# Optimization experiments

Measured on AMD Instinct MI355X. Metric: run time of the kernel, lower is better.

The kernel has to match this reference:

```python
import jax, jax.numpy as jnp
import numpy as np

MIN_SIGMA = 0.001


def setup_inputs() -> dict:
    key = jax.random.key(0)
    kA, kB = jax.random.split(key)
    A = jax.random.normal(kA, (8, 2048, 128), dtype=jnp.float32)
    B = jax.random.normal(kB, (4096, 128), dtype=jnp.float32)
    sigma = jnp.float32(1.0)
    return {"A": A, "B": B, "sigma": sigma}


def reference(A, B, sigma):
    # A: (bs, n, d), B: (m, d) -> K: (bs, n, m)
    A_norm = jnp.sum(A * A, axis=-1, keepdims=True)          # (bs, n, 1)
    B_norm = jnp.sum(B * B, axis=-1)[None, None, :]          # (1, 1, m)
    AB = jnp.einsum('bnd,md->bnm', A, B)                     # (bs, n, m)
    dist2 = jnp.maximum(A_norm + B_norm - 2.0 * AB, 0.0)
    sig = jnp.maximum(sigma, MIN_SIGMA)
    K = jnp.exp(-dist2 / (2.0 * sig * sig))
    return K
```

## Files before the change

### kernel.cpp

```cpp
#include <hip/hip_runtime.h>


typedef __attribute__((ext_vector_type(8))) short bf16x8;
typedef __attribute__((ext_vector_type(4))) float f32x4;

#define NROW_A 16384
#define NROW_B 4096
#define D      128

#define OFF_AHI 0u
#define OFF_BHI (OFF_AHI + NROW_A * D * 2u)
#define OFF_NA  (OFF_BHI + NROW_B * D * 2u)
#define OFF_NB  (OFF_NA + NROW_A * 4u)
#define WS_NEED (OFF_NB + NROW_B * 4u)

#define BAR_LDS() do { asm volatile("s_waitcnt lgkmcnt(0)" ::: "memory"); \
                       __builtin_amdgcn_s_barrier(); } while (0)

__device__ __forceinline__ short f2bf_hi(float x) {
    union { float f; unsigned u; } v; v.f = x;
    unsigned r = (v.u + 0x7fffu + ((v.u >> 16) & 1u)) >> 16;
    return (short)r;
}
__device__ __forceinline__ float bf2f(short h) {
    union { unsigned u; float f; } v; v.u = ((unsigned)(unsigned short)h) << 16;
    return v.f;
}

__global__ __launch_bounds__(256)
void rbf_precompute(const float* __restrict__ A, const float* __restrict__ Bm,
                    short* __restrict__ Ahi, short* __restrict__ Bhi,
                    float* __restrict__ nA, float* __restrict__ nB) {
    const int g   = blockIdx.x * 256 + threadIdx.x;
    const int row = g >> 4;
    const int c   = g & 15;

    const float* src; short* dhi; float* nrm; int r;
    if (row < NROW_A) {
        r = row; src = A + (size_t)r * D;
        dhi = Ahi + (size_t)r * D; nrm = nA + r;
    } else {
        r = row - NROW_A; src = Bm + (size_t)r * D;
        dhi = Bhi + (size_t)r * D; nrm = nB + r;
    }

    float4 v0 = *(const float4*)(src + c * 8);
    float4 v1 = *(const float4*)(src + c * 8 + 4);
    float f[8] = {v0.x, v0.y, v0.z, v0.w, v1.x, v1.y, v1.z, v1.w};

    bf16x8 hi;
    float ss = 0.0f;
#pragma unroll
    for (int e = 0; e < 8; ++e) {
        hi[e] = f2bf_hi(f[e]);
        ss += f[e] * f[e];
    }
    *(bf16x8*)(dhi + c * 8) = hi;

#pragma unroll
    for (int m = 1; m <= 8; m <<= 1) ss += __shfl_xor(ss, m);
    if (c == 0) *nrm = ss;
}

__global__ __launch_bounds__(512, 4)
void rbf_mfma_persist(const short* __restrict__ Ahi, const short* __restrict__ Bhi,
                      const float* __restrict__ nAg, const float* __restrict__ nBg,
                      const float* __restrict__ sigp, float* __restrict__ out) {
    __shared__ __align__(16) short sA[128 * 128];
    __shared__ __align__(16) short sB[128 * 128];

    const int tid = threadIdx.x;
    const int bid = blockIdx.x;
    const int xcd = bid & 7;
    const int idx = bid >> 3;
    const int bcol = ((xcd << 2) + (idx & 3)) << 7;
    const int bg   = idx >> 2;

    const int srow = tid >> 2;
    const int sc4  = tid & 3;

    const int lane = tid & 63;
    const int w    = tid >> 6;
    const int wr   = (w >> 1) << 5;
    const int wc   = (w & 1) << 6;
    const int lr   = lane & 15;
    const int kb   = lane >> 4;

#pragma unroll
    for (int it = 0; it < 4; ++it) {
        const int c  = sc4 + (it << 2);
        const int cs = c ^ (srow & 15);
        *(bf16x8*)&sB[srow * 128 + cs * 8] =
            *(const bf16x8*)&Bhi[(size_t)(bcol + srow) * D + c * 8];
    }
    const int brow0 = (bg << 3) << 7;
#pragma unroll
    for (int it = 0; it < 4; ++it) {
        const int c  = sc4 + (it << 2);
        const int cs = c ^ (srow & 15);
        *(bf16x8*)&sA[srow * 128 + cs * 8] =
            *(const bf16x8*)&Ahi[(size_t)(brow0 + srow) * D + c * 8];
    }

    f32x4 nb[4];
#pragma unroll
    for (int j = 0; j < 4; ++j)
        nb[j] = *(const f32x4*)&nBg[bcol + wc + (j << 4) + (kb << 2)];

    float nac0 = nAg[brow0 + wr + lr];
    float nac1 = nAg[brow0 + wr + 16 + lr];

    float sg = fmaxf(sigp[0], 0.001f);
    const float cc = -0.5f / (sg * sg);

    __syncthreads();

    bf16x8 rh[4];
    float nan0 = 0.0f, nan1 = 0.0f;

    for (int t = 0; t < 8; ++t) {
        const int browt = ((bg << 3) + t) << 7;

        if (t < 7) {
            const int brn = browt + 128;
            nan0 = nAg[brn + wr + lr];
            nan1 = nAg[brn + wr + 16 + lr];
#pragma unroll
            for (int it = 0; it < 4; ++it) {
                const int c = sc4 + (it << 2);
                rh[it] = *(const bf16x8*)&Ahi[(size_t)(brn + srow) * D + c * 8];
            }
        }

        f32x4 acc[2][4] = {};
#pragma unroll
        for (int ks = 0; ks < 4; ++ks) {
            const int off = (((ks << 2) + kb) ^ lr) << 3;
            bf16x8 af[2], bf[4];
#pragma unroll
            for (int i = 0; i < 2; ++i)
                af[i] = *(const bf16x8*)&sA[(wr + (i << 4) + lr) * 128 + off];
#pragma unroll
            for (int j = 0; j < 4; ++j)
                bf[j] = *(const bf16x8*)&sB[(wc + (j << 4) + lr) * 128 + off];
#pragma unroll
            for (int i = 0; i < 2; ++i)
#pragma unroll
                for (int j = 0; j < 4; ++j)
                    acc[i][j] = __builtin_amdgcn_mfma_f32_16x16x32_bf16(bf[j], af[i], acc[i][j], 0, 0, 0);
        }

#pragma unroll
        for (int i = 0; i < 2; ++i) {
            const int orow = browt + wr + (i << 4) + lr;
            const float na = i ? nac1 : nac0;
#pragma unroll
            for (int j = 0; j < 4; ++j) {
                const int ocol = wc + (j << 4) + (kb << 2);
                f32x4 v;
#pragma unroll
                for (int r = 0; r < 4; ++r) {
                    float d2 = fmaxf(na + nb[j][r] - 2.0f * acc[i][j][r], 0.0f);
                    v[r] = __expf(d2 * cc);
                }
                *(f32x4*)(out + (size_t)orow * 4096 + bcol + ocol) = v;
            }
        }

        if (t < 7) {
            BAR_LDS();
#pragma unroll
            for (int it = 0; it < 4; ++it) {
                const int c  = sc4 + (it << 2);
                const int cs = c ^ (srow & 15);
                *(bf16x8*)&sA[srow * 128 + cs * 8] = rh[it];
            }
            BAR_LDS();
            nac0 = nan0;
            nac1 = nan1;
        }
    }
}

#define PK 136
__global__ __launch_bounds__(256, 2)
void rbf_mfma_fallback(const float* __restrict__ A, const float* __restrict__ Bm,
                       const float* __restrict__ sigp, float* __restrict__ out) {
    __shared__ __align__(16) short sAhi[64 * PK];
    __shared__ __align__(16) short sAlo[64 * PK];
    __shared__ __align__(16) short sBhi[64 * PK];
    __shared__ __align__(16) short sBlo[64 * PK];
    __shared__ float nA[64];
    __shared__ float nB[64];

    const int tid  = threadIdx.x;
    const int brow = blockIdx.y << 6;
    const int bcol = blockIdx.x << 6;

    const int r0 = tid >> 5;
    const int kq = (tid & 31) << 2;
#pragma unroll
    for (int it = 0; it < 8; ++it) {
        const int row = r0 + (it << 3);
        const float4 va = *(const float4*)(A  + (size_t)(brow + row) * 128 + kq);
        const float4 vb = *(const float4*)(Bm + (size_t)(bcol + row) * 128 + kq);
        short4 ha, la, hb, lb;
        ha.x = f2bf_hi(va.x); la.x = f2bf_hi(va.x - bf2f(ha.x));
        ha.y = f2bf_hi(va.y); la.y = f2bf_hi(va.y - bf2f(ha.y));
        ha.z = f2bf_hi(va.z); la.z = f2bf_hi(va.z - bf2f(ha.z));
        ha.w = f2bf_hi(va.w); la.w = f2bf_hi(va.w - bf2f(ha.w));
        hb.x = f2bf_hi(vb.x); lb.x = f2bf_hi(vb.x - bf2f(hb.x));
        hb.y = f2bf_hi(vb.y); lb.y = f2bf_hi(vb.y - bf2f(hb.y));
        hb.z = f2bf_hi(vb.z); lb.z = f2bf_hi(vb.z - bf2f(hb.z));
        hb.w = f2bf_hi(vb.w); lb.w = f2bf_hi(vb.w - bf2f(hb.w));
        const int idx = row * PK + kq;
        *(short4*)(&sAhi[idx]) = ha;
        *(short4*)(&sAlo[idx]) = la;
        *(short4*)(&sBhi[idx]) = hb;
        *(short4*)(&sBlo[idx]) = lb;
        float sa = va.x * va.x + va.y * va.y + va.z * va.z + va.w * va.w;
        float sb = vb.x * vb.x + vb.y * vb.y + vb.z * vb.z + vb.w * vb.w;
#pragma unroll
        for (int m = 16; m >= 1; m >>= 1) { sa += __shfl_xor(sa, m); sb += __shfl_xor(sb, m); }
        if ((tid & 31) == 0) { nA[row] = sa; nB[row] = sb; }
    }
    __syncthreads();

    const int lane = tid & 63;
    const int w    = tid >> 6;
    const int wr   = (w >> 1) << 5;
    const int wc   = (w & 1) << 5;
    const int lr   = lane & 15;
    const int kb   = lane >> 4;
    f32x4 acc[2][2] = {};
#pragma unroll
    for (int ks = 0; ks < 4; ++ks) {
        const int kc = (ks << 5) + (kb << 3);
        bf16x8 ahi[2], alo[2], bhi[2], blo[2];
#pragma unroll
        for (int i = 0; i < 2; ++i) {
            const int ar = (wr + (i << 4) + lr) * PK + kc;
            ahi[i] = *(const bf16x8*)(&sAhi[ar]);
            alo[i] = *(const bf16x8*)(&sAlo[ar]);
            const int br = (wc + (i << 4) + lr) * PK + kc;
            bhi[i] = *(const bf16x8*)(&sBhi[br]);
            blo[i] = *(const bf16x8*)(&sBlo[br]);
        }
#pragma unroll
        for (int i = 0; i < 2; ++i)
#pragma unroll
            for (int j = 0; j < 2; ++j) {
                acc[i][j] = __builtin_amdgcn_mfma_f32_16x16x32_bf16(ahi[i], bhi[j], acc[i][j], 0, 0, 0);
                acc[i][j] = __builtin_amdgcn_mfma_f32_16x16x32_bf16(ahi[i], blo[j], acc[i][j], 0, 0, 0);
                acc[i][j] = __builtin_amdgcn_mfma_f32_16x16x32_bf16(alo[i], bhi[j], acc[i][j], 0, 0, 0);
            }
    }
    float sg = fmaxf(sigp[0], 0.001f);
    const float c = -0.5f / (sg * sg);
#pragma unroll
    for (int i = 0; i < 2; ++i)
#pragma unroll
        for (int j = 0; j < 2; ++j)
#pragma unroll
            for (int r = 0; r < 4; ++r) {
                const int lrow = wr + (i << 4) + (kb << 2) + r;
                const int lcol = wc + (j << 4) + lr;
                float d2 = nA[lrow] + nB[lcol] - 2.0f * acc[i][j][r];
                d2 = fmaxf(d2, 0.0f);
                out[(size_t)(brow + lrow) * 4096 + (bcol + lcol)] = __expf(d2 * c);
            }
}

extern "C" void kernel_launch(void* const* d_in, const int* in_sizes, int n_in,
                              void* d_out, int out_size, void* d_ws, size_t ws_size,
                              hipStream_t stream) {
    const float* A    = (const float*)d_in[0];
    const float* Bm   = (const float*)d_in[1];
    const float* sigp = (const float*)d_in[2];
    float* out = (float*)d_out;

    if (ws_size >= WS_NEED) {
        char* ws = (char*)d_ws;
        short* Ahi = (short*)(ws + OFF_AHI);
        short* Bhi = (short*)(ws + OFF_BHI);
        float* nA  = (float*)(ws + OFF_NA);
        float* nB  = (float*)(ws + OFF_NB);

        dim3 pgrid((NROW_A + NROW_B) * 16 / 256, 1, 1);
        rbf_precompute<<<pgrid, 256, 0, stream>>>(A, Bm, Ahi, Bhi, nA, nB);

        rbf_mfma_persist<<<dim3(512, 1, 1), dim3(512, 1, 1), 0, stream>>>(
            Ahi, Bhi, nA, nB, sigp, out);
    } else {
        dim3 grid(4096 / 64, 16384 / 64, 1);
        rbf_mfma_fallback<<<grid, dim3(256, 1, 1), 0, stream>>>(A, Bm, sigp, out);
    }
}
```

Before: 60.75 us.

## Load A fragments directly from global into registers, drop A LDS staging

The persistent MFMA kernel no longer stages A tiles through shared memory. Each wave now loads its own A fragments straight from global memory into registers, prefetching the next tile right after the MFMAs. This removes the per-tile LDS writes and both barriers, and halves LDS use, which may allow higher occupancy. In exchange, A rows read by several waves are fetched redundantly from global/L2, and the prefetch now overwrites the fragment registers after the MFMA loop, so less of the load latency is hidden.

```diff
diff --git a/kernel.cpp b/kernel.cpp
--- a/kernel.cpp
+++ b/kernel.cpp
@@ -13,9 +13,6 @@
 #define OFF_NA  (OFF_BHI + NROW_B * D * 2u)
 #define OFF_NB  (OFF_NA + NROW_A * 4u)
 #define WS_NEED (OFF_NB + NROW_B * 4u)
-
-#define BAR_LDS() do { asm volatile("s_waitcnt lgkmcnt(0)" ::: "memory"); \
-                       __builtin_amdgcn_s_barrier(); } while (0)
 
 __device__ __forceinline__ short f2bf_hi(float x) {
     union { float f; unsigned u; } v; v.f = x;
@@ -66,7 +63,6 @@
 void rbf_mfma_persist(const short* __restrict__ Ahi, const short* __restrict__ Bhi,
                       const float* __restrict__ nAg, const float* __restrict__ nBg,
                       const float* __restrict__ sigp, float* __restrict__ out) {
-    __shared__ __align__(16) short sA[128 * 128];
     __shared__ __align__(16) short sB[128 * 128];
 
     const int tid = threadIdx.x;
@@ -93,20 +89,20 @@
         *(bf16x8*)&sB[srow * 128 + cs * 8] =
             *(const bf16x8*)&Bhi[(size_t)(bcol + srow) * D + c * 8];
     }
-    const int brow0 = (bg << 3) << 7;
-#pragma unroll
-    for (int it = 0; it < 4; ++it) {
-        const int c  = sc4 + (it << 2);
-        const int cs = c ^ (srow & 15);
-        *(bf16x8*)&sA[srow * 128 + cs * 8] =
-            *(const bf16x8*)&Ahi[(size_t)(brow0 + srow) * D + c * 8];
-    }
 
     f32x4 nb[4];
 #pragma unroll
     for (int j = 0; j < 4; ++j)
         nb[j] = *(const f32x4*)&nBg[bcol + wc + (j << 4) + (kb << 2)];
 
+    bf16x8 af[8];
+    const int brow0 = (bg << 3) << 7;
+#pragma unroll
+    for (int ks = 0; ks < 4; ++ks) {
+        const int koff = ((ks << 2) + kb) << 3;
+        af[ks * 2 + 0] = *(const bf16x8*)&Ahi[(size_t)(brow0 + wr + lr) * D + koff];
+        af[ks * 2 + 1] = *(const bf16x8*)&Ahi[(size_t)(brow0 + wr + 16 + lr) * D + koff];
+    }
     float nac0 = nAg[brow0 + wr + lr];
     float nac1 = nAg[brow0 + wr + 16 + lr];
 
@@ -115,39 +111,35 @@
 
     __syncthreads();
 
-    bf16x8 rh[4];
-    float nan0 = 0.0f, nan1 = 0.0f;
-
     for (int t = 0; t < 8; ++t) {
         const int browt = ((bg << 3) + t) << 7;
 
+        f32x4 acc[2][4] = {};
+#pragma unroll
+        for (int ks = 0; ks < 4; ++ks) {
+            const int off = (((ks << 2) + kb) ^ lr) << 3;
+            bf16x8 bf[4];
+#pragma unroll
+            for (int j = 0; j < 4; ++j)
+                bf[j] = *(const bf16x8*)&sB[(wc + (j << 4) + lr) * 128 + off];
+#pragma unroll
+            for (int i = 0; i < 2; ++i)
+#pragma unroll
+                for (int j = 0; j < 4; ++j)
+                    acc[i][j] = __builtin_amdgcn_mfma_f32_16x16x32_bf16(bf[j], af[ks * 2 + i], acc[i][j], 0, 0, 0);
+        }
+
+        float nan0 = 0.0f, nan1 = 0.0f;
         if (t < 7) {
             const int brn = browt + 128;
+#pragma unroll
+            for (int ks = 0; ks < 4; ++ks) {
+                const int koff = ((ks << 2) + kb) << 3;
+                af[ks * 2 + 0] = *(const bf16x8*)&Ahi[(size_t)(brn + wr + lr) * D + koff];
+                af[ks * 2 + 1] = *(const bf16x8*)&Ahi[(size_t)(brn + wr + 16 + lr) * D + koff];
+            }
             nan0 = nAg[brn + wr + lr];
             nan1 = nAg[brn + wr + 16 + lr];
-#pragma unroll
-            for (int it = 0; it < 4; ++it) {
-                const int c = sc4 + (it << 2);
-                rh[it] = *(const bf16x8*)&Ahi[(size_t)(brn + srow) * D + c * 8];
-            }
-        }
-
-        f32x4 acc[2][4] = {};
-#pragma unroll
-        for (int ks = 0; ks < 4; ++ks) {
-            const int off = (((ks << 2) + kb) ^ lr) << 3;
-            bf16x8 af[2], bf[4];
-#pragma unroll
-            for (int i = 0; i < 2; ++i)
-                af[i] = *(const bf16x8*)&sA[(wr + (i << 4) + lr) * 128 + off];
-#pragma unroll
-            for (int j = 0; j < 4; ++j)
-                bf[j] = *(const bf16x8*)&sB[(wc + (j << 4) + lr) * 128 + off];
-#pragma unroll
-            for (int i = 0; i < 2; ++i)
-#pragma unroll
-                for (int j = 0; j < 4; ++j)
-                    acc[i][j] = __builtin_amdgcn_mfma_f32_16x16x32_bf16(bf[j], af[i], acc[i][j], 0, 0, 0);
         }
 
 #pragma unroll
@@ -167,18 +159,8 @@
             }
         }
 
-        if (t < 7) {
-            BAR_LDS();
-#pragma unroll
-            for (int it = 0; it < 4; ++it) {
-                const int c  = sc4 + (it << 2);
-                const int cs = c ^ (srow & 15);
-                *(bf16x8*)&sA[srow * 128 + cs * 8] = rh[it];
-            }
-            BAR_LDS();
-            nac0 = nan0;
-            nac1 = nan1;
-        }
+        nac0 = nan0;
+        nac1 = nan1;
     }
 }
 
```

Result: slower. 123.1 us (+102.7%).
